# Kernel tuning notes

Measured on AMD Instinct MI355X. Metric: run time of the kernel, lower is better.

The kernel has to match this reference:

```python
import jax, jax.numpy as jnp
import numpy as np

B, S, D_MODEL = 4, 4096, 2048
D_SPACE = 128
N_C, N_QK, N_V = 512, 512, 512
TOPK_C, TOPK_QK, TOPK_V = 8, 4, 6


def setup_inputs() -> dict:
    key = jax.random.key(0)
    k1, k2, k3, k4 = jax.random.split(key, 4)
    x = jax.random.normal(k1, (B, S, D_MODEL), dtype=jnp.float32)
    importance = jax.random.uniform(k2, (B, S), dtype=jnp.float32)
    proj_w = jax.random.normal(k3, (D_SPACE, D_MODEL), dtype=jnp.float32) * (1.0 / np.sqrt(D_MODEL))
    proj_b = jnp.zeros((D_SPACE,), dtype=jnp.float32)
    neuron_emb = jax.random.normal(k4, (N_C + N_QK + N_V, D_SPACE), dtype=jnp.float32) * 0.02
    return {"x": x, "importance": importance, "proj_w": proj_w, "proj_b": proj_b, "neuron_emb": neuron_emb}


def _topk_sparsify(w, k):
    # torch: topk -> scatter into zeros -> renormalize
    vals, idx = jax.lax.top_k(w, k)                      # [B,k]
    b = jnp.arange(w.shape[0])[:, None]
    sparse = jnp.zeros_like(w).at[b, idx].set(vals)      # [B,n]
    return sparse / (sparse.sum(axis=-1, keepdims=True) + 1e-8)


def reference(x, importance, proj_w, proj_b, neuron_emb):
    # eval mode: dropout off, no starvation bonus, no EMA / aux loss
    h = jnp.einsum("bsd,ed->bse", x, proj_w) + proj_b          # [B,S,d_space]
    nrm = jnp.linalg.norm(neuron_emb, axis=-1, keepdims=True)
    emb_n = neuron_emb / jnp.maximum(nrm, 1e-12)               # F.normalize
    logits = jnp.einsum("bse,ne->bsn", h, emb_n)               # [B,S,total]

    log_c = logits[..., :N_C]
    log_qk = logits[..., N_C:N_C + N_QK]                        # expand_Q == expand_K slice
    log_v = logits[..., N_C + N_QK:]

    pref_c = jax.nn.softmax(log_c, axis=-1)
    pref_qk = jax.nn.softmax(log_qk, axis=-1)
    pref_v = jax.nn.softmax(log_v, axis=-1)

    dense_c = jnp.einsum("bs,bsn->bn", importance, pref_c)
    dense_qk = jnp.einsum("bs,bsn->bn", importance, pref_qk)
    dense_v = jnp.einsum("bs,bsn->bn", importance, pref_v)

    cw = _topk_sparsify(dense_c, TOPK_C)
    qw = _topk_sparsify(dense_qk, TOPK_QK)   # Q and K use identical logits in eval
    kw = _topk_sparsify(dense_qk, TOPK_QK)
    vw = _topk_sparsify(dense_v, TOPK_V)
    return jnp.stack([cw, qw, kw, vw])       # [4, B, 512]
```

## Files before the change

### kernel.cpp

```cpp
#include <hip/hip_runtime.h>
#include <hip/hip_bf16.h>

#define BATCH 4
#define S_TOT 4096
#define ROWS (BATCH * S_TOT)
#define DM 2048
#define DSP 128
#define NSEG 512

typedef short short8 __attribute__((ext_vector_type(8)));
typedef float f32x16 __attribute__((ext_vector_type(16)));

static __device__ inline short f2bf(float v, float& back) {
  unsigned u = __float_as_uint(v);
  unsigned r = u + 0x7FFFu + ((u >> 16) & 1u);
  unsigned short hs = (unsigned short)(r >> 16);
  back = __uint_as_float(((unsigned)hs) << 16);
  return (short)hs;
}


__global__ __launch_bounds__(64) void k0_norm(const float* __restrict__ emb,
                                              short* __restrict__ eHi,
                                              short* __restrict__ eLo) {
  const int row = blockIdx.x;
  const int l = threadIdx.x;
  __shared__ short sh[128], sl[128];
  float2 v = *(const float2*)&emb[row * 128 + l * 2];
  float ss = v.x * v.x + v.y * v.y;
  #pragma unroll
  for (int m = 32; m; m >>= 1) ss += __shfl_xor(ss, m);
  const float inv = 1.0f / fmaxf(sqrtf(ss), 1e-12f);
  float bk;
  const float ox = v.x * inv, oy = v.y * inv;
  sh[2 * l] = f2bf(ox, bk);     sl[2 * l] = f2bf(ox - bk, bk);
  sh[2 * l + 1] = f2bf(oy, bk); sl[2 * l + 1] = f2bf(oy - bk, bk);
  __syncthreads();
  if (l < 32) {
    const int split = l >> 4, kc = (l >> 1) & 7, kh = l & 1;
    const short* src = (split ? sl : sh) + kc * 16 + kh * 8;
    const short8 val = *(const short8*)src;
    const size_t idx = (size_t)(row >> 5) * 4096 + kc * 512 +
                       ((row & 31) + 32 * kh) * 8;
    *(short8*)((split ? eLo : eHi) + idx) = val;
  }
}

__global__ __launch_bounds__(512, 2) void k1_mfma(const float* __restrict__ x,
                                                  const float* __restrict__ W,
                                                  const float* __restrict__ bias,
                                                  float* __restrict__ h0,
                                                  float* __restrict__ h1) {
  __shared__ __align__(16) short lds[2][4][4][128][8];

  const int t = threadIdx.x;
  const int m0 = blockIdx.x * 128;
  const int y = blockIdx.y;
  const int kb0 = y * 1024;

  const int sr = t >> 2;
  const int skg = t & 3;
  const float* xp = x + (size_t)(m0 + sr) * DM + kb0 + skg * 8;
  const float* wp = W + (size_t)sr * DM + kb0 + skg * 8;

  const int wave = t >> 6;
  const int lane = t & 63;
  const int wr = wave >> 1;
  const int wc = wave & 1;
  const int fr = lane & 31;
  const int ks = lane >> 5;

  f32x16 acc0 = {}; f32x16 acc1 = {};

  #define STAGE(buf, step)                                                      \
    {                                                                           \
      const int off = (step) * 32;                                              \
      float4 a0 = *(const float4*)(xp + off);                                   \
      float4 a1 = *(const float4*)(xp + off + 4);                               \
      float4 b0 = *(const float4*)(wp + off);                                   \
      float4 b1 = *(const float4*)(wp + off + 4);                               \
      short8 ah, al, bh, bl; float bk;                                          \
      const float av[8] = {a0.x,a0.y,a0.z,a0.w,a1.x,a1.y,a1.z,a1.w};            \
      const float bv[8] = {b0.x,b0.y,b0.z,b0.w,b1.x,b1.y,b1.z,b1.w};            \
      _Pragma("unroll")                                                         \
      for (int e = 0; e < 8; ++e) {                                             \
        ah[e] = f2bf(av[e], bk); al[e] = f2bf(av[e] - bk, bk);                  \
      }                                                                         \
      _Pragma("unroll")                                                         \
      for (int e = 0; e < 8; ++e) {                                             \
        bh[e] = f2bf(bv[e], bk); bl[e] = f2bf(bv[e] - bk, bk);                  \
      }                                                                         \
      *(short8*)&lds[buf][0][skg][sr][0] = ah;                                  \
      *(short8*)&lds[buf][1][skg][sr][0] = al;                                  \
      *(short8*)&lds[buf][2][skg][sr][0] = bh;                                  \
      *(short8*)&lds[buf][3][skg][sr][0] = bl;                                  \
    }

  #define COMPUTE(buf)                                                          \
    {                                                                           \
      _Pragma("unroll")                                                         \
      for (int kh = 0; kh < 2; ++kh) {                                          \
        const int kg = kh * 2 + ks;                                             \
        short8 ahf = *(const short8*)&lds[buf][0][kg][wr * 32 + fr][0];         \
        short8 alf = *(const short8*)&lds[buf][1][kg][wr * 32 + fr][0];         \
        short8 bh0 = *(const short8*)&lds[buf][2][kg][wc * 64 + fr][0];         \
        short8 bl0 = *(const short8*)&lds[buf][3][kg][wc * 64 + fr][0];         \
        short8 bh1 = *(const short8*)&lds[buf][2][kg][wc * 64 + 32 + fr][0];    \
        short8 bl1 = *(const short8*)&lds[buf][3][kg][wc * 64 + 32 + fr][0];    \
        acc0 = __builtin_amdgcn_mfma_f32_32x32x16_bf16(ahf, bh0, acc0, 0, 0, 0);\
        acc0 = __builtin_amdgcn_mfma_f32_32x32x16_bf16(ahf, bl0, acc0, 0, 0, 0);\
        acc0 = __builtin_amdgcn_mfma_f32_32x32x16_bf16(alf, bh0, acc0, 0, 0, 0);\
        acc1 = __builtin_amdgcn_mfma_f32_32x32x16_bf16(ahf, bh1, acc1, 0, 0, 0);\
        acc1 = __builtin_amdgcn_mfma_f32_32x32x16_bf16(ahf, bl1, acc1, 0, 0, 0);\
        acc1 = __builtin_amdgcn_mfma_f32_32x32x16_bf16(alf, bh1, acc1, 0, 0, 0);\
      }                                                                         \
    }

  STAGE(0, 0);
  __syncthreads();
  #pragma unroll 1
  for (int s = 0; s < 32; ++s) {
    if (s + 1 < 32) STAGE((s + 1) & 1, s + 1);
    COMPUTE(s & 1);
    __syncthreads();
  }

  float* hq = y ? h1 : h0;
  #pragma unroll
  for (int reg = 0; reg < 16; ++reg) {
    const int row = (reg & 3) + 8 * (reg >> 2) + 4 * ks;
    const int gr = m0 + wr * 32 + row;
    const int gc0 = wc * 64 + fr;
    const int gc1 = wc * 64 + 32 + fr;
    float v0 = acc0[reg], v1 = acc1[reg];
    if (y == 0) { v0 += bias[gc0]; v1 += bias[gc1]; }
    hq[(size_t)gr * DSP + gc0] = v0;
    hq[(size_t)gr * DSP + gc1] = v1;
  }
  #undef STAGE
  #undef COMPUTE
}

__global__ __launch_bounds__(256) void k1b_pack(const float* __restrict__ h0,
                                                const float* __restrict__ h1,
                                                short* __restrict__ hHi,
                                                short* __restrict__ hLo) {
  const int t = threadIdx.x;
  const int row = blockIdx.x * 16 + (t >> 4);
  const int c = t & 15;
  const float4* p0 = (const float4*)(h0 + (size_t)row * 128 + c * 8);
  const float4* p1 = (const float4*)(h1 + (size_t)row * 128 + c * 8);
  const float4 a0 = p0[0], a1 = p0[1], b0 = p1[0], b1 = p1[1];
  const float v[8] = {a0.x + b0.x, a0.y + b0.y, a0.z + b0.z, a0.w + b0.w,
                      a1.x + b1.x, a1.y + b1.y, a1.z + b1.z, a1.w + b1.w};
  short8 hiv, lov; float bk;
  #pragma unroll
  for (int e = 0; e < 8; ++e) {
    hiv[e] = f2bf(v[e], bk); lov[e] = f2bf(v[e] - bk, bk);
  }
  const int kc = c >> 1, kh = c & 1;
  const size_t idx = (size_t)(row >> 5) * 4096 + kc * 512 +
                     ((row & 31) + 32 * kh) * 8;
  *(short8*)(hHi + idx) = hiv;
  *(short8*)(hLo + idx) = lov;
}

__global__ __launch_bounds__(512, 2) void k2_mfma(const short* __restrict__ hHi,
                                                  const short* __restrict__ hLo,
                                                  const short* __restrict__ eHi,
                                                  const short* __restrict__ eLo,
                                                  const float* __restrict__ imp,
                                                  float* __restrict__ partials) {
  const int t = threadIdx.x;
  const int m0 = blockIdx.x * 64;
  const int seg = blockIdx.y;
  const int wave = t >> 6, lane = t & 63;
  const int wr = wave >> 2;
  const int wc = wave & 3;
  const int fr = lane & 31;
  const int hi = lane >> 5;

  __shared__ float redA[2][32][4];
  __shared__ float redB[2][32][4];
  __shared__ float ldsD[2][512];

  f32x16 acc[4] = {};

  const short8* pAh = (const short8*)hHi + ((m0 >> 5) + wr) * 512 + lane;
  const short8* pAl = (const short8*)hLo + ((m0 >> 5) + wr) * 512 + lane;
  const short8* pBh = (const short8*)eHi + (seg * 16 + wc * 4) * 512 + lane;
  const short8* pBl = (const short8*)eLo + (seg * 16 + wc * 4) * 512 + lane;

  #pragma unroll
  for (int kc = 0; kc < 8; ++kc) {
    const short8 ah = pAh[kc * 64];
    const short8 al = pAl[kc * 64];
    #pragma unroll
    for (int t2 = 0; t2 < 4; ++t2) {
      const short8 bh = pBh[t2 * 512 + kc * 64];
      const short8 bl = pBl[t2 * 512 + kc * 64];
      acc[t2] = __builtin_amdgcn_mfma_f32_32x32x16_bf16(ah, bh, acc[t2], 0, 0, 0);
      acc[t2] = __builtin_amdgcn_mfma_f32_32x32x16_bf16(ah, bl, acc[t2], 0, 0, 0);
      acc[t2] = __builtin_amdgcn_mfma_f32_32x32x16_bf16(al, bh, acc[t2], 0, 0, 0);
    }
  }

  float mx[16];
  #pragma unroll
  for (int r = 0; r < 16; ++r) {
    float m = fmaxf(fmaxf(acc[0][r], acc[1][r]), fmaxf(acc[2][r], acc[3][r]));
    #pragma unroll
    for (int k = 1; k < 32; k <<= 1) m = fmaxf(m, __shfl_xor(m, k));
    mx[r] = m;
  }
  if (fr == 0) {
    #pragma unroll
    for (int r = 0; r < 16; ++r)
      redA[wr][(r & 3) + 8 * (r >> 2) + 4 * hi][wc] = mx[r];
  }
  __syncthreads();
  float M[16];
  #pragma unroll
  for (int r = 0; r < 16; ++r) {
    const int row = (r & 3) + 8 * (r >> 2) + 4 * hi;
    M[r] = fmaxf(fmaxf(redA[wr][row][0], redA[wr][row][1]),
                 fmaxf(redA[wr][row][2], redA[wr][row][3]));
  }

  float sm[16];
  #pragma unroll
  for (int r = 0; r < 16; ++r) {
    float s = 0.0f;
    #pragma unroll
    for (int t2 = 0; t2 < 4; ++t2) {
      const float p = __expf(acc[t2][r] - M[r]);
      acc[t2][r] = p;
      s += p;
    }
    #pragma unroll
    for (int k = 1; k < 32; k <<= 1) s += __shfl_xor(s, k);
    sm[r] = s;
  }
  if (fr == 0) {
    #pragma unroll
    for (int r = 0; r < 16; ++r)
      redB[wr][(r & 3) + 8 * (r >> 2) + 4 * hi][wc] = sm[r];
  }
  __syncthreads();
  float w[16];
  #pragma unroll
  for (int r = 0; r < 16; ++r) {
    const int row = (r & 3) + 8 * (r >> 2) + 4 * hi;
    const float S = (redB[wr][row][0] + redB[wr][row][1]) +
                    (redB[wr][row][2] + redB[wr][row][3]);
    w[r] = imp[m0 + wr * 32 + row] / S;
  }

  #pragma unroll
  for (int t2 = 0; t2 < 4; ++t2) {
    float d = 0.0f;
    #pragma unroll
    for (int r = 0; r < 16; ++r) d = fmaf(acc[t2][r], w[r], d);
    d += __shfl_xor(d, 32);
    if (hi == 0) ldsD[wr][wc * 128 + t2 * 32 + fr] = d;
  }
  __syncthreads();
  partials[((size_t)seg * 256 + blockIdx.x) * 512 + t] = ldsD[0][t] + ldsD[1][t];
}

__global__ __launch_bounds__(256) void k3_topk(const float* __restrict__ partials,
                                               float* __restrict__ out) {
  const int b = blockIdx.x;
  const int seg = blockIdx.y;
  const int tid = threadIdx.x;
  const int K = (seg == 0) ? 8 : ((seg == 1) ? 4 : 6);

  __shared__ float v[512];
  __shared__ float wv[8];
  __shared__ int wi[8];
  __shared__ float redv[4];
  __shared__ int redi[4];

  const float* src = partials + ((size_t)seg * 256 + b * 64) * 512;
  float a0 = 0.0f, a1 = 0.0f;
  for (int j = 0; j < 64; ++j) {
    a0 += src[(size_t)j * 512 + tid];
    a1 += src[(size_t)j * 512 + tid + 256];
  }
  v[tid] = a0;
  v[tid + 256] = a1;
  __syncthreads();

  for (int t = 0; t < K; ++t) {
    const float v0 = v[tid], v1 = v[tid + 256];
    float bv; int bi;
    if (v1 > v0) { bv = v1; bi = tid + 256; } else { bv = v0; bi = tid; }
    #pragma unroll
    for (int m = 1; m < 64; m <<= 1) {
      const float ov = __shfl_xor(bv, m);
      const int oi = __shfl_xor(bi, m);
      if (ov > bv || (ov == bv && oi < bi)) { bv = ov; bi = oi; }
    }
    if ((tid & 63) == 0) { redv[tid >> 6] = bv; redi[tid >> 6] = bi; }
    __syncthreads();
    if (tid == 0) {
      float best = redv[0]; int besti = redi[0];
      for (int q = 1; q < 4; ++q)
        if (redv[q] > best || (redv[q] == best && redi[q] < besti)) {
          best = redv[q]; besti = redi[q];
        }
      wv[t] = best; wi[t] = besti;
      v[besti] = -3.0e38f;
    }
    __syncthreads();
  }

  float s = 1e-8f;
  for (int t = 0; t < K; ++t) s += wv[t];

  const int slot0 = (seg == 0) ? 0 : ((seg == 1) ? 1 : 3);
  float* o0 = out + slot0 * (BATCH * NSEG) + b * NSEG;
  o0[tid] = 0.0f; o0[tid + 256] = 0.0f;
  float* o1 = nullptr;
  if (seg == 1) {
    o1 = out + 2 * (BATCH * NSEG) + b * NSEG;
    o1[tid] = 0.0f; o1[tid + 256] = 0.0f;
  }
  __syncthreads();
  if (tid < K) {
    const float val = wv[tid] / s;
    o0[wi[tid]] = val;
    if (seg == 1) o1[wi[tid]] = val;
  }
}

extern "C" void kernel_launch(void* const* d_in, const int* in_sizes, int n_in,
                              void* d_out, int out_size, void* d_ws, size_t ws_size,
                              hipStream_t stream) {
  (void)in_sizes; (void)n_in; (void)out_size; (void)ws_size;
  const float* x    = (const float*)d_in[0];
  const float* imp  = (const float*)d_in[1];
  const float* W    = (const float*)d_in[2];
  const float* bias = (const float*)d_in[3];
  const float* emb  = (const float*)d_in[4];
  float* out = (float*)d_out;

  float* h0       = (float*)d_ws;
  float* h1       = h0 + 2097152;
  float* partials = h1 + 2097152;
  short* hHi      = (short*)(partials + 768 * 512);
  short* hLo      = hHi + 2097152;
  short* eHi      = hLo + 2097152;
  short* eLo      = eHi + 196608;

  k0_norm<<<1536, 64, 0, stream>>>(emb, eHi, eLo);
  k1_mfma<<<dim3(ROWS / 128, 2), 512, 0, stream>>>(x, W, bias, h0, h1);
  k1b_pack<<<ROWS / 16, 256, 0, stream>>>(h0, h1, hHi, hLo);
  k2_mfma<<<dim3(ROWS / 64, 3), 512, 0, stream>>>(hHi, hLo, eHi, eLo, imp, partials);
  k3_topk<<<dim3(BATCH, 3), 256, 0, stream>>>(partials, out);
}
```

Measured before the change: 114.2 us.

## Pre-split W to bf16 once and fuse projection GEMM with hi/lo packing

The projection weight W is now split into bf16 hi/lo fragments once, in a prep kernel merged with the embedding normalization. The projection GEMM is restructured so each block handles 32 rows with a 4-way K-split across waves, loading B fragments directly from global memory and reducing the partial sums in LDS. Bias add and hi/lo packing of h happen in the same kernel, which removes the fp32 h0/h1 round trip and the separate pack kernel. The top-k partial-sum loop also gains multiple accumulators for more memory-level parallelism. The trade-off is that B is read from global/L2 without LDS reuse, and the block shape is smaller.

```diff
diff --git a/kernel.cpp b/kernel.cpp
--- a/kernel.cpp
+++ b/kernel.cpp
@@ -20,149 +20,145 @@
 }
 
 
-__global__ __launch_bounds__(64) void k0_norm(const float* __restrict__ emb,
+__global__ __launch_bounds__(64) void k0_prep(const float* __restrict__ W,
+                                              const float* __restrict__ emb,
+                                              short* __restrict__ wHi,
+                                              short* __restrict__ wLo,
                                               short* __restrict__ eHi,
                                               short* __restrict__ eLo) {
-  const int row = blockIdx.x;
   const int l = threadIdx.x;
-  __shared__ short sh[128], sl[128];
-  float2 v = *(const float2*)&emb[row * 128 + l * 2];
-  float ss = v.x * v.x + v.y * v.y;
-  #pragma unroll
-  for (int m = 32; m; m >>= 1) ss += __shfl_xor(ss, m);
-  const float inv = 1.0f / fmaxf(sqrtf(ss), 1e-12f);
-  float bk;
-  const float ox = v.x * inv, oy = v.y * inv;
-  sh[2 * l] = f2bf(ox, bk);     sl[2 * l] = f2bf(ox - bk, bk);
-  sh[2 * l + 1] = f2bf(oy, bk); sl[2 * l + 1] = f2bf(oy - bk, bk);
-  __syncthreads();
-  if (l < 32) {
-    const int split = l >> 4, kc = (l >> 1) & 7, kh = l & 1;
-    const short* src = (split ? sl : sh) + kc * 16 + kh * 8;
-    const short8 val = *(const short8*)src;
-    const size_t idx = (size_t)(row >> 5) * 4096 + kc * 512 +
-                       ((row & 31) + 32 * kh) * 8;
-    *(short8*)((split ? eLo : eHi) + idx) = val;
-  }
-}
-
-__global__ __launch_bounds__(512, 2) void k1_mfma(const float* __restrict__ x,
-                                                  const float* __restrict__ W,
-                                                  const float* __restrict__ bias,
-                                                  float* __restrict__ h0,
-                                                  float* __restrict__ h1) {
-  __shared__ __align__(16) short lds[2][4][4][128][8];
-
+  if (blockIdx.x < 512) {
+    const int tc = blockIdx.x;
+    const int t = tc >> 7, c = tc & 127;
+    const int n = t * 32 + (l & 31);
+    const int k = c * 16 + (l >> 5) * 8;
+    const float4 a0 = *(const float4*)&W[(size_t)n * DM + k];
+    const float4 a1 = *(const float4*)&W[(size_t)n * DM + k + 4];
+    const float av[8] = {a0.x, a0.y, a0.z, a0.w, a1.x, a1.y, a1.z, a1.w};
+    short8 hi8, lo8; float bk;
+    #pragma unroll
+    for (int e = 0; e < 8; ++e) {
+      hi8[e] = f2bf(av[e], bk); lo8[e] = f2bf(av[e] - bk, bk);
+    }
+    const size_t idx = (size_t)tc * 64 + l;
+    ((short8*)wHi)[idx] = hi8;
+    ((short8*)wLo)[idx] = lo8;
+  } else {
+    const int row = blockIdx.x - 512;
+    __shared__ short sh[128], sl[128];
+    float2 v = *(const float2*)&emb[row * 128 + l * 2];
+    float ss = v.x * v.x + v.y * v.y;
+    #pragma unroll
+    for (int m = 32; m; m >>= 1) ss += __shfl_xor(ss, m);
+    const float inv = 1.0f / fmaxf(sqrtf(ss), 1e-12f);
+    float bk;
+    const float ox = v.x * inv, oy = v.y * inv;
+    sh[2 * l] = f2bf(ox, bk);     sl[2 * l] = f2bf(ox - bk, bk);
+    sh[2 * l + 1] = f2bf(oy, bk); sl[2 * l + 1] = f2bf(oy - bk, bk);
+    __syncthreads();
+    if (l < 32) {
+      const int split = l >> 4, kc = (l >> 1) & 7, kh = l & 1;
+      const short* src = (split ? sl : sh) + kc * 16 + kh * 8;
+      const short8 val = *(const short8*)src;
+      const size_t idx = (size_t)(row >> 5) * 4096 + kc * 512 +
+                         ((row & 31) + 32 * kh) * 8;
+      *(short8*)((split ? eLo : eHi) + idx) = val;
+    }
+  }
+}
+
+__global__ __launch_bounds__(256, 3) void k1_fused(const float* __restrict__ x,
+                                                   const short* __restrict__ wHi,
+                                                   const short* __restrict__ wLo,
+                                                   const float* __restrict__ bias,
+                                                   short* __restrict__ hHi,
+                                                   short* __restrict__ hLo) {
+  __shared__ __align__(16) float hsA[32][132];
+  __shared__ __align__(16) float hsB[32][132];
+  __shared__ float bsh[128];
   const int t = threadIdx.x;
-  const int m0 = blockIdx.x * 128;
-  const int y = blockIdx.y;
-  const int kb0 = y * 1024;
-
-  const int sr = t >> 2;
-  const int skg = t & 3;
-  const float* xp = x + (size_t)(m0 + sr) * DM + kb0 + skg * 8;
-  const float* wp = W + (size_t)sr * DM + kb0 + skg * 8;
-
-  const int wave = t >> 6;
-  const int lane = t & 63;
-  const int wr = wave >> 1;
-  const int wc = wave & 1;
-  const int fr = lane & 31;
-  const int ks = lane >> 5;
-
-  f32x16 acc0 = {}; f32x16 acc1 = {};
-
-  #define STAGE(buf, step)                                                      \
-    {                                                                           \
-      const int off = (step) * 32;                                              \
-      float4 a0 = *(const float4*)(xp + off);                                   \
-      float4 a1 = *(const float4*)(xp + off + 4);                               \
-      float4 b0 = *(const float4*)(wp + off);                                   \
-      float4 b1 = *(const float4*)(wp + off + 4);                               \
-      short8 ah, al, bh, bl; float bk;                                          \
-      const float av[8] = {a0.x,a0.y,a0.z,a0.w,a1.x,a1.y,a1.z,a1.w};            \
-      const float bv[8] = {b0.x,b0.y,b0.z,b0.w,b1.x,b1.y,b1.z,b1.w};            \
-      _Pragma("unroll")                                                         \
-      for (int e = 0; e < 8; ++e) {                                             \
-        ah[e] = f2bf(av[e], bk); al[e] = f2bf(av[e] - bk, bk);                  \
-      }                                                                         \
-      _Pragma("unroll")                                                         \
-      for (int e = 0; e < 8; ++e) {                                             \
-        bh[e] = f2bf(bv[e], bk); bl[e] = f2bf(bv[e] - bk, bk);                  \
-      }                                                                         \
-      *(short8*)&lds[buf][0][skg][sr][0] = ah;                                  \
-      *(short8*)&lds[buf][1][skg][sr][0] = al;                                  \
-      *(short8*)&lds[buf][2][skg][sr][0] = bh;                                  \
-      *(short8*)&lds[buf][3][skg][sr][0] = bl;                                  \
-    }
-
-  #define COMPUTE(buf)                                                          \
-    {                                                                           \
-      _Pragma("unroll")                                                         \
-      for (int kh = 0; kh < 2; ++kh) {                                          \
-        const int kg = kh * 2 + ks;                                             \
-        short8 ahf = *(const short8*)&lds[buf][0][kg][wr * 32 + fr][0];         \
-        short8 alf = *(const short8*)&lds[buf][1][kg][wr * 32 + fr][0];         \
-        short8 bh0 = *(const short8*)&lds[buf][2][kg][wc * 64 + fr][0];         \
-        short8 bl0 = *(const short8*)&lds[buf][3][kg][wc * 64 + fr][0];         \
-        short8 bh1 = *(const short8*)&lds[buf][2][kg][wc * 64 + 32 + fr][0];    \
-        short8 bl1 = *(const short8*)&lds[buf][3][kg][wc * 64 + 32 + fr][0];    \
-        acc0 = __builtin_amdgcn_mfma_f32_32x32x16_bf16(ahf, bh0, acc0, 0, 0, 0);\
-        acc0 = __builtin_amdgcn_mfma_f32_32x32x16_bf16(ahf, bl0, acc0, 0, 0, 0);\
-        acc0 = __builtin_amdgcn_mfma_f32_32x32x16_bf16(alf, bh0, acc0, 0, 0, 0);\
-        acc1 = __builtin_amdgcn_mfma_f32_32x32x16_bf16(ahf, bh1, acc1, 0, 0, 0);\
-        acc1 = __builtin_amdgcn_mfma_f32_32x32x16_bf16(ahf, bl1, acc1, 0, 0, 0);\
-        acc1 = __builtin_amdgcn_mfma_f32_32x32x16_bf16(alf, bh1, acc1, 0, 0, 0);\
-      }                                                                         \
-    }
-
-  STAGE(0, 0);
-  __syncthreads();
-  #pragma unroll 1
-  for (int s = 0; s < 32; ++s) {
-    if (s + 1 < 32) STAGE((s + 1) & 1, s + 1);
-    COMPUTE(s & 1);
-    __syncthreads();
-  }
-
-  float* hq = y ? h1 : h0;
-  #pragma unroll
-  for (int reg = 0; reg < 16; ++reg) {
-    const int row = (reg & 3) + 8 * (reg >> 2) + 4 * ks;
-    const int gr = m0 + wr * 32 + row;
-    const int gc0 = wc * 64 + fr;
-    const int gc1 = wc * 64 + 32 + fr;
-    float v0 = acc0[reg], v1 = acc1[reg];
-    if (y == 0) { v0 += bias[gc0]; v1 += bias[gc1]; }
-    hq[(size_t)gr * DSP + gc0] = v0;
-    hq[(size_t)gr * DSP + gc1] = v1;
-  }
-  #undef STAGE
-  #undef COMPUTE
-}
-
-__global__ __launch_bounds__(256) void k1b_pack(const float* __restrict__ h0,
-                                                const float* __restrict__ h1,
-                                                short* __restrict__ hHi,
-                                                short* __restrict__ hLo) {
-  const int t = threadIdx.x;
-  const int row = blockIdx.x * 16 + (t >> 4);
-  const int c = t & 15;
-  const float4* p0 = (const float4*)(h0 + (size_t)row * 128 + c * 8);
-  const float4* p1 = (const float4*)(h1 + (size_t)row * 128 + c * 8);
-  const float4 a0 = p0[0], a1 = p0[1], b0 = p1[0], b1 = p1[1];
-  const float v[8] = {a0.x + b0.x, a0.y + b0.y, a0.z + b0.z, a0.w + b0.w,
-                      a1.x + b1.x, a1.y + b1.y, a1.z + b1.z, a1.w + b1.w};
-  short8 hiv, lov; float bk;
-  #pragma unroll
-  for (int e = 0; e < 8; ++e) {
-    hiv[e] = f2bf(v[e], bk); lov[e] = f2bf(v[e] - bk, bk);
-  }
-  const int kc = c >> 1, kh = c & 1;
-  const size_t idx = (size_t)(row >> 5) * 4096 + kc * 512 +
-                     ((row & 31) + 32 * kh) * 8;
-  *(short8*)(hHi + idx) = hiv;
-  *(short8*)(hLo + idx) = lov;
+  const int wave = t >> 6, lane = t & 63;
+  const int fr = lane & 31, ks = lane >> 5;
+  const int m0 = blockIdx.x * 32;
+
+  if (t < 128) bsh[t] = bias[t];
+
+  const float* xp = x + (size_t)(m0 + fr) * DM + wave * 512 + ks * 8;
+  const short8* bhp = (const short8*)wHi;
+  const short8* blp = (const short8*)wLo;
+
+  f32x16 acc[4] = {};
+
+  #pragma unroll 2
+  for (int c = 0; c < 32; ++c) {
+    const int cc = wave * 32 + c;
+    const float4 a0 = *(const float4*)(xp + c * 16);
+    const float4 a1 = *(const float4*)(xp + c * 16 + 4);
+    const float av[8] = {a0.x, a0.y, a0.z, a0.w, a1.x, a1.y, a1.z, a1.w};
+    short8 ah, al; float bk;
+    #pragma unroll
+    for (int e = 0; e < 8; ++e) {
+      ah[e] = f2bf(av[e], bk); al[e] = f2bf(av[e] - bk, bk);
+    }
+    const short8* bb = bhp + (size_t)cc * 64 + lane;
+    const short8* bb2 = blp + (size_t)cc * 64 + lane;
+    #pragma unroll
+    for (int t2 = 0; t2 < 4; ++t2) {
+      const short8 bh = bb[t2 * 8192];
+      const short8 bl = bb2[t2 * 8192];
+      acc[t2] = __builtin_amdgcn_mfma_f32_32x32x16_bf16(ah, bh, acc[t2], 0, 0, 0);
+      acc[t2] = __builtin_amdgcn_mfma_f32_32x32x16_bf16(ah, bl, acc[t2], 0, 0, 0);
+      acc[t2] = __builtin_amdgcn_mfma_f32_32x32x16_bf16(al, bh, acc[t2], 0, 0, 0);
+    }
+  }
+
+  if (wave == 0 || wave == 1) {
+    float (*hs)[132] = wave ? hsB : hsA;
+    #pragma unroll
+    for (int t2 = 0; t2 < 4; ++t2)
+      #pragma unroll
+      for (int reg = 0; reg < 16; ++reg) {
+        const int row = (reg & 3) + 8 * (reg >> 2) + 4 * ks;
+        hs[row][t2 * 32 + fr] = acc[t2][reg];
+      }
+  }
+  __syncthreads();
+  if (wave == 2 || wave == 3) {
+    float (*hs)[132] = (wave == 3) ? hsB : hsA;
+    #pragma unroll
+    for (int t2 = 0; t2 < 4; ++t2)
+      #pragma unroll
+      for (int reg = 0; reg < 16; ++reg) {
+        const int row = (reg & 3) + 8 * (reg >> 2) + 4 * ks;
+        hs[row][t2 * 32 + fr] += acc[t2][reg];
+      }
+  }
+  __syncthreads();
+
+  #pragma unroll
+  for (int i = 0; i < 2; ++i) {
+    const int task = t + 256 * i;
+    const int row = task >> 4, kc8 = task & 15;
+    const float4 va = *(const float4*)&hsA[row][kc8 * 8];
+    const float4 vb = *(const float4*)&hsA[row][kc8 * 8 + 4];
+    const float4 wa = *(const float4*)&hsB[row][kc8 * 8];
+    const float4 wb = *(const float4*)&hsB[row][kc8 * 8 + 4];
+    const float4 ba = *(const float4*)&bsh[kc8 * 8];
+    const float4 bb4 = *(const float4*)&bsh[kc8 * 8 + 4];
+    const float v[8] = {va.x + wa.x + ba.x, va.y + wa.y + ba.y,
+                        va.z + wa.z + ba.z, va.w + wa.w + ba.w,
+                        vb.x + wb.x + bb4.x, vb.y + wb.y + bb4.y,
+                        vb.z + wb.z + bb4.z, vb.w + wb.w + bb4.w};
+    short8 hi8, lo8; float bk;
+    #pragma unroll
+    for (int e = 0; e < 8; ++e) {
+      hi8[e] = f2bf(v[e], bk); lo8[e] = f2bf(v[e] - bk, bk);
+    }
+    const int kc = kc8 >> 1, kh = kc8 & 1;
+    const size_t idx = (size_t)blockIdx.x * 512 + kc * 64 + (row + 32 * kh);
+    ((short8*)hHi)[idx] = hi8;
+    ((short8*)hLo)[idx] = lo8;
+  }
 }
 
 __global__ __launch_bounds__(512, 2) void k2_mfma(const short* __restrict__ hHi,
@@ -282,13 +278,20 @@
   __shared__ int redi[4];
 
   const float* src = partials + ((size_t)seg * 256 + b * 64) * 512;
-  float a0 = 0.0f, a1 = 0.0f;
-  for (int j = 0; j < 64; ++j) {
-    a0 += src[(size_t)j * 512 + tid];
-    a1 += src[(size_t)j * 512 + tid + 256];
-  }
-  v[tid] = a0;
-  v[tid + 256] = a1;
+  float a0 = 0.f, a1 = 0.f, a2 = 0.f, a3 = 0.f;
+  float b0 = 0.f, b1 = 0.f, b2 = 0.f, b3 = 0.f;
+  for (int j = 0; j < 64; j += 4) {
+    a0 += src[(size_t)(j + 0) * 512 + tid];
+    a1 += src[(size_t)(j + 1) * 512 + tid];
+    a2 += src[(size_t)(j + 2) * 512 + tid];
+    a3 += src[(size_t)(j + 3) * 512 + tid];
+    b0 += src[(size_t)(j + 0) * 512 + tid + 256];
+    b1 += src[(size_t)(j + 1) * 512 + tid + 256];
+    b2 += src[(size_t)(j + 2) * 512 + tid + 256];
+    b3 += src[(size_t)(j + 3) * 512 + tid + 256];
+  }
+  v[tid] = (a0 + a1) + (a2 + a3);
+  v[tid + 256] = (b0 + b1) + (b2 + b3);
   __syncthreads();
 
   for (int t = 0; t < K; ++t) {
@@ -345,17 +348,16 @@
   const float* emb  = (const float*)d_in[4];
   float* out = (float*)d_out;
 
-  float* h0       = (float*)d_ws;
-  float* h1       = h0 + 2097152;
-  float* partials = h1 + 2097152;
+  float* partials = (float*)d_ws;
   short* hHi      = (short*)(partials + 768 * 512);
   short* hLo      = hHi + 2097152;
   short* eHi      = hLo + 2097152;
   short* eLo      = eHi + 196608;
-
-  k0_norm<<<1536, 64, 0, stream>>>(emb, eHi, eLo);
-  k1_mfma<<<dim3(ROWS / 128, 2), 512, 0, stream>>>(x, W, bias, h0, h1);
-  k1b_pack<<<ROWS / 16, 256, 0, stream>>>(h0, h1, hHi, hLo);
+  short* wHi      = eLo + 196608;
+  short* wLo      = wHi + 262144;
+
+  k0_prep<<<512 + 1536, 64, 0, stream>>>(W, emb, wHi, wLo, eHi, eLo);
+  k1_fused<<<ROWS / 32, 256, 0, stream>>>(x, wHi, wLo, bias, hHi, hLo);
   k2_mfma<<<dim3(ROWS / 64, 3), 512, 0, stream>>>(hHi, hLo, eHi, eLo, imp, partials);
   k3_topk<<<dim3(BATCH, 3), 256, 0, stream>>>(partials, out);
 }
```

After: 120.9 us. 5.9% more time.
